# Kernel tuning notes

Hardware: AMD Instinct MI355X
Metric: run time of the kernel (lower is better)

Reference implementation:

```python
import jax, jax.numpy as jnp
import numpy as np

T, B, H, W, D, N, M, A = 48, 16, 16, 48, 684, 256, 256, 512
CQ, KQ, PAD = 512, 11, 5  # coverage conv: 1->512 channels, 11x11, pad 5


def setup_inputs() -> dict:
    key = jax.random.key(0)
    ks = iter(jax.random.split(key, 40))
    w = lambda *s: jax.random.normal(next(ks), s, jnp.float32) * 0.05
    inp = {
        "embedding": jax.random.normal(next(ks), (T, B, M), jnp.float32),
        "mask": jnp.ones((T, B), jnp.float32),
        "context": jax.random.normal(next(ks), (B, D, H, W), jnp.float32),
        "context_mask": jnp.ones((B, H, W), jnp.float32),
        "init_state": jax.random.normal(next(ks), (B, N), jnp.float32),
        # attention params
        "Ua_w": w(A, D), "Ua_b": w(A),              # conv_Ua (1x1 conv == linear over channels)
        "Wa_w": w(A, N),                              # fc_Wa (no bias)
        "Q_w": w(CQ, 1, KQ, KQ),                      # conv_Q (no bias)
        "Uf_w": w(A, CQ), "Uf_b": w(A),               # fc_Uf
        "va_w": w(1, A), "va_b": w(1),                # fc_va
        # GRU 1 (input-driven)
        "Wyz_w": w(N, M), "Wyz_b": w(N),
        "Wyr_w": w(N, M), "Wyr_b": w(N),
        "Wyh_w": w(N, M), "Wyh_b": w(N),
        "Uhz_w": w(N, N), "Uhr_w": w(N, N), "Uhh_w": w(N, N),
        # GRU 2 (context-driven)
        "Wcz_w": w(N, D), "Wcr_w": w(N, D), "Wch_w": w(N, D),
        "Uhz2_w": w(N, N), "Uhz2_b": w(N),
        "Uhr2_w": w(N, N), "Uhr2_b": w(N),
        "Uhh2_w": w(N, N), "Uhh2_b": w(N),
    }
    return inp


def reference(embedding, mask, context, context_mask, init_state,
              Ua_w, Ua_b, Wa_w, Q_w, Uf_w, Uf_b, va_w, va_b,
              Wyz_w, Wyz_b, Wyr_w, Wyr_b, Wyh_w, Wyh_b,
              Uhz_w, Uhr_w, Uhh_w, Wcz_w, Wcr_w, Wch_w,
              Uhz2_w, Uhz2_b, Uhr2_w, Uhr2_b, Uhh2_w, Uhh2_b):
    # Precompute, as the torch module does, the context projection and
    # embedding projections for all steps.
    Ua_ctx = jnp.einsum('bdhw,ad->hwba', context, Ua_w) + Ua_b   # [H,W,B,A]
    sz = jnp.einsum('tbm,nm->tbn', embedding, Wyz_w) + Wyz_b     # [T,B,N]
    sr = jnp.einsum('tbm,nm->tbn', embedding, Wyr_w) + Wyr_b
    sh = jnp.einsum('tbm,nm->tbn', embedding, Wyh_w) + Wyh_b
    ctx_mask_hwb = jnp.transpose(context_mask, (1, 2, 0))        # [H,W,B]
    nb = context.shape[0]
    alpha_past0 = jnp.zeros((nb, context.shape[2], context.shape[3]), context.dtype)

    def step(carry, xs):
        h, ap = carry
        m_t, sz_t, sr_t, sh_t = xs
        # GRU 1
        z1 = jax.nn.sigmoid(h @ Uhz_w.T + sz_t)
        r1 = jax.nn.sigmoid(h @ Uhr_w.T + sr_t)
        h1p = jnp.tanh((h @ Uhh_w.T) * r1 + sh_t)
        h1 = z1 * h + (1.0 - z1) * h1p
        h1 = m_t[:, None] * h1 + (1.0 - m_t)[:, None] * h
        # coverage-conv attention
        Wa_h1 = h1 @ Wa_w.T                                      # [B,A]
        cf = jax.lax.conv_general_dilated(
            ap[:, None], Q_w, (1, 1), [(PAD, PAD), (PAD, PAD)],
            dimension_numbers=('NCHW', 'OIHW', 'NCHW'))          # [B,CQ,H,W]
        cover = jnp.einsum('bchw,ac->hwba', cf, Uf_w) + Uf_b     # [H,W,B,A]
        att = jnp.tanh(Ua_ctx + Wa_h1[None, None] + cover)
        e = jnp.einsum('hwba,a->hwb', att, va_w[0]) + va_b[0]
        alpha = jnp.exp(e) * ctx_mask_hwb
        alpha = alpha / alpha.sum(axis=(0, 1))[None, None, :]    # normalize over H,W
        a_bhw = jnp.transpose(alpha, (2, 0, 1))
        ap_new = ap + a_bhw
        ct = jnp.einsum('bdhw,bhw->bd', context, a_bhw)          # [B,D]
        # GRU 2
        z2 = jax.nn.sigmoid(ct @ Wcz_w.T + h1 @ Uhz2_w.T + Uhz2_b)
        r2 = jax.nn.sigmoid(ct @ Wcr_w.T + h1 @ Uhr2_w.T + Uhr2_b)
        h2p = jnp.tanh(ct @ Wch_w.T + (h1 @ Uhh2_w.T + Uhh2_b) * r2)
        h2 = z2 * h1 + (1.0 - z2) * h2p
        h2 = m_t[:, None] * h2 + (1.0 - m_t)[:, None] * h1
        return (h2, ap_new), (h2, ct, a_bhw, ap_new)

    _, (h2ts, cts, alphas, alpha_pasts) = jax.lax.scan(
        step, (init_state, alpha_past0), (mask, sz, sr, sh))
    return h2ts, cts, alphas, alpha_pasts
```

## Files before the change

### kernel.cpp

```cpp
#include <hip/hip_runtime.h>
#include <hip/hip_bf16.h>
#include <stdint.h>

#define T_  48
#define B_  16
#define HW_ 768
#define D_  684
#define N_  256
#define A_  512

#define OFF_SZ     0u
#define OFF_SR     196608u
#define OFF_SH     393216u
#define OFF_UHZT   589824u
#define OFF_UHZ2T  786432u
#define OFF_G2HP   983040u
#define OFF_WAT    1179648u
#define OFF_WCZT   1310720u
#define OFF_UAB    1836032u
#define OFF_WAHP   2012160u
#define OFF_H1     2077696u
#define OFF_KCB    2186240u
#define OFF_G2CT   2219008u
#define OFF_AP     2275008u
#define OFF_AUN    2287296u
#define OFF_UACTX  2299584u

#define OUT_H2 0u
#define OUT_CT 196608u
#define OUT_AL 721920u
#define OUT_AP 1311744u

typedef __attribute__((ext_vector_type(8))) short bf16x8;
typedef __attribute__((ext_vector_type(16))) float floatx16;

__device__ __forceinline__ float sigf(float x)  { return 1.f / (1.f + __expf(-x)); }
__device__ __forceinline__ float tanhf_(float x){ float e = __expf(2.f*x); return 1.f - 2.f/(e + 1.f); }
__device__ __forceinline__ float bfval(unsigned short u){ return __uint_as_float(((unsigned)u) << 16); }
__device__ __forceinline__ unsigned short f2bf(float f){
  unsigned int x = __float_as_uint(f);
  return (unsigned short)((x + 0x7fffu + ((x >> 16) & 1u)) >> 16);
}

__global__ void k_prep(const float* __restrict__ Uhz, const float* __restrict__ Uhr, const float* __restrict__ Uhh,
                       const float* __restrict__ Uhz2, const float* __restrict__ Uhr2, const float* __restrict__ Uhh2,
                       const float* __restrict__ Wyz, const float* __restrict__ Wyr, const float* __restrict__ Wyh,
                       const float* __restrict__ Wa, const float* __restrict__ Wcz, const float* __restrict__ Wcr,
                       const float* __restrict__ Wch, const float* __restrict__ Ua, float* __restrict__ ws)
{
  int i = blockIdx.x * 256 + threadIdx.x;
  if (i < 589824) {
    int m = i >> 16, rem = i & 65535, r = rem >> 8, c = rem & 255;
    const float* s;
    unsigned dst;
    switch (m) { case 0: s=Uhz;  dst=OFF_UHZT;           break;
                 case 1: s=Uhr;  dst=OFF_UHZT+65536u;    break;
                 case 2: s=Uhh;  dst=OFF_UHZT+131072u;   break;
                 case 3: s=Uhz2; dst=OFF_UHZ2T;          break;
                 case 4: s=Uhr2; dst=OFF_UHZ2T+65536u;   break;
                 case 5: s=Uhh2; dst=OFF_UHZ2T+131072u;  break;
                 case 6: s=Wyz;  dst=983040u;            break;
                 case 7: s=Wyr;  dst=1048576u;           break;
                 default: s=Wyh; dst=1114112u;           break;}
    ws[dst + c*256 + r] = s[rem];
  } else if (i < 720896) {
    int j = i - 589824, r = j >> 8, c = j & 255;
    ws[OFF_WAT + c*512 + r] = Wa[j];
  } else if (i < 1246208) {
    int j = i - 720896; int m = j / 175104; int rem = j - m*175104;
    int r = rem / 684, c = rem - r*684;
    const float* s = (m == 0) ? Wcz : (m == 1) ? Wcr : Wch;
    ws[OFF_WCZT + m*175104 + c*256 + r] = s[rem];
  } else if (i < 1596416) {
    int j = i - 1246208; int a = j / 684, d = j - a*684;
    unsigned short* uab = (unsigned short*)(ws + OFF_UAB);
    uab[(size_t)a*688 + d] = f2bf(Ua[j]);
  } else if (i < 1598464) {
    int j = i - 1596416; int a = j >> 2, d = 684 + (j & 3);
    unsigned short* uab = (unsigned short*)(ws + OFF_UAB);
    uab[(size_t)a*688 + d] = 0;
  } else if (i < 1610752) {
    ws[OFF_AP + (i - 1598464)] = 0.f;
  }
}

__global__ void __launch_bounds__(256) k_kcomb(const float* __restrict__ Uf, const float* __restrict__ Qw,
                                               float* __restrict__ ws)
{
  unsigned short* kcb = (unsigned short*)(ws + OFF_KCB);
  int tid = threadIdx.x;
  int k = tid & 127, rr = tid >> 7;
  int a = blockIdx.x * 2 + rr;
  if (k >= 121) { kcb[(size_t)a*128 + k] = 0; return; }
  const float* uf = Uf + (size_t)a*512;
  float acc = 0.f;
  #pragma unroll 8
  for (int c = 0; c < 512; ++c) acc += uf[c] * Qw[c*121 + k];
  kcb[(size_t)a*128 + k] = f2bf(acc);
}

__global__ void k_embproj(const float* __restrict__ emb, const float* __restrict__ bz,
                          const float* __restrict__ br, const float* __restrict__ bh,
                          float* __restrict__ ws)
{
  __shared__ __align__(16) float s_e[256 * 16];
  int tid = threadIdx.x, row0 = blockIdx.x * 16;
  for (int i = tid; i < 4096; i += 256) { int r = i >> 8, m = i & 255; s_e[m*16 + r] = emb[(row0 + r)*256 + m]; }
  __syncthreads();
  int n = tid;
  float az[16], arr[16], ahh[16];
  float vz = bz[n], vr = br[n], vh = bh[n];
  #pragma unroll
  for (int r = 0; r < 16; ++r) { az[r] = vz; arr[r] = vr; ahh[r] = vh; }
  for (int m = 0; m < 256; ++m) {
    float wz = ws[983040u + m*256 + n];
    float wr = ws[1048576u + m*256 + n];
    float wh = ws[1114112u + m*256 + n];
    #pragma unroll
    for (int r = 0; r < 16; ++r) { float e = s_e[m*16 + r]; az[r] += wz*e; arr[r] += wr*e; ahh[r] += wh*e; }
  }
  #pragma unroll
  for (int r = 0; r < 16; ++r) {
    int ro = (row0 + r)*256 + n;
    ws[OFF_SZ + ro] = az[r]; ws[OFF_SR + ro] = arr[r]; ws[OFF_SH + ro] = ahh[r];
  }
}

__global__ void __launch_bounds__(256) k_uactx(const float* __restrict__ ctx, float* __restrict__ ws)
{
  __shared__ unsigned short sA[32 * 24];
  int tid = threadIdx.x;
  int blk = blockIdx.x;
  int b = blk / 48; int r2 = blk % 48; int ch = r2 >> 1; int ah = r2 & 1;
  int hw0 = ch * 32;
  const unsigned short* uab = (const unsigned short*)(ws + OFF_UAB);
  int lane = tid & 63, w = tid >> 6;
  int c5 = lane & 31, q = lane >> 5;
  int nb = ah*256 + w*64;
  floatx16 acc[2];
  #pragma unroll
  for (int nt = 0; nt < 2; ++nt)
    #pragma unroll
    for (int r = 0; r < 16; ++r) acc[nt][r] = 0.f;
  int dd = tid >> 4, iw = tid & 15;
  for (int kt = 0; kt < 43; ++kt) {
    int d = kt*16 + dd;
    float2 v = {0.f, 0.f};
    if (d < 684) v = *(const float2*)(ctx + ((size_t)(b*684 + d))*768 + hw0 + iw*2);
    __syncthreads();
    sA[(iw*2 + 0)*24 + dd] = f2bf(v.x);
    sA[(iw*2 + 1)*24 + dd] = f2bf(v.y);
    __syncthreads();
    bf16x8 af = *(const bf16x8*)(sA + c5*24 + q*8);
    #pragma unroll
    for (int nt = 0; nt < 2; ++nt) {
      bf16x8 bf = *(const bf16x8*)(uab + (size_t)(nb + nt*32 + c5)*688 + kt*16 + q*8);
      acc[nt] = __builtin_amdgcn_mfma_f32_32x32x16_bf16(af, bf, acc[nt], 0, 0, 0);
    }
  }
  unsigned short* up = (unsigned short*)(ws + OFF_UACTX);
  #pragma unroll
  for (int nt = 0; nt < 2; ++nt) {
    int col = nb + nt*32 + c5;
    #pragma unroll
    for (int r = 0; r < 16; ++r) {
      int row32 = (r & 3) + 8*(r >> 2) + 4*q;
      int hw = hw0 + row32;
      up[((size_t)(b*768 + hw))*512 + col] = f2bf(acc[nt][r]);
    }
  }
}

__global__ void __launch_bounds__(256) k_step0(const float* __restrict__ inits, const float* __restrict__ maskp,
                                               float* __restrict__ ws)
{
  __shared__ float s_h[256];
  __shared__ float s_part[3][8][32];
  __shared__ float s_h1[32];
  int tid = threadIdx.x;
  int b = blockIdx.x >> 3, q = blockIdx.x & 7;
  s_h[tid] = inits[b*256 + tid];
  if (q == 0) {
    for (int i = tid; i < 768; i += 256) ws[OFF_AUN + b*768 + i] = 0.f;
    #pragma unroll
    for (int g = 0; g < 3; ++g) ws[OFF_G2CT + (b*3 + g)*256 + tid] = 0.f;
  }
  __syncthreads();
  {
    int nl = tid & 31, kq = tid >> 5;
    int col = q*32 + nl;
    const float* Wz = ws + OFF_UHZT;
    const float* Wr = ws + OFF_UHZT + 65536u;
    const float* Wh = ws + OFF_UHZT + 131072u;
    float a0 = 0.f, a1 = 0.f, a2 = 0.f;
    #pragma unroll 8
    for (int k = kq*32; k < kq*32 + 32; ++k) {
      float hk = s_h[k];
      a0 += Wz[k*256 + col]*hk; a1 += Wr[k*256 + col]*hk; a2 += Wh[k*256 + col]*hk;
    }
    s_part[0][kq][nl] = a0; s_part[1][kq][nl] = a1; s_part[2][kq][nl] = a2;
  }
  __syncthreads();
  if (tid < 32) {
    float g0 = 0.f, g1 = 0.f, g2 = 0.f;
    #pragma unroll
    for (int j = 0; j < 8; ++j) { g0 += s_part[0][j][tid]; g1 += s_part[1][j][tid]; g2 += s_part[2][j][tid]; }
    int col = q*32 + tid;
    int ro = b*256 + col;
    float z1 = sigf(g0 + ws[OFF_SZ + ro]);
    float r1 = sigf(g1 + ws[OFF_SR + ro]);
    float h1p = tanhf_(g2 * r1 + ws[OFF_SH + ro]);
    float m = maskp[b];
    float h = s_h[col];
    float h1 = m*(z1*h + (1.f - z1)*h1p) + (1.f - m)*h;
    s_h1[tid] = h1;
    ws[OFF_H1 + b*256 + col] = h1;
  }
  __syncthreads();
  {
    float acc0 = 0.f, acc1 = 0.f;
    #pragma unroll 8
    for (int j = 0; j < 32; ++j) {
      float h1j = s_h1[j];
      acc0 += ws[OFF_WAT + (q*32 + j)*512 + tid]       * h1j;
      acc1 += ws[OFF_WAT + (q*32 + j)*512 + tid + 256] * h1j;
    }
    ws[OFF_WAHP + (size_t)(b*8 + q)*512 + tid]       = acc0;
    ws[OFF_WAHP + (size_t)(b*8 + q)*512 + tid + 256] = acc1;
  }
  #pragma unroll
  for (int g = 0; g < 3; ++g) {
    const float* Wb = ws + OFF_UHZ2T + g*65536u;
    float acc = 0.f;
    #pragma unroll 8
    for (int j = 0; j < 32; ++j) acc += Wb[(q*32 + j)*256 + tid] * s_h1[j];
    ws[OFF_G2HP + (size_t)((b*8 + q)*3 + g)*256 + tid] = acc;
  }
}

__global__ void __launch_bounds__(256) k_step1(int t, const float* __restrict__ maskp,
                                               const float* __restrict__ bz2, const float* __restrict__ br2,
                                               const float* __restrict__ bh2,
                                               float* __restrict__ out, float* __restrict__ ws)
{
  __shared__ float s_h[256];
  __shared__ float s_part[3][8][32];
  __shared__ float s_h1[32];
  int tid = threadIdx.x;
  int b = blockIdx.x >> 3, q = blockIdx.x & 7;
  const unsigned pr = (unsigned)((t - 1) & 1);
  const unsigned pw = (unsigned)(t & 1);
  {
    int n = tid;
    float h1v = ws[OFF_H1 + pr*4096u + b*256 + n];
    float gz = ws[OFF_G2CT + pr*12288u + (b*3 + 0)*256 + n];
    float gr = ws[OFF_G2CT + pr*12288u + (b*3 + 1)*256 + n];
    float gc = ws[OFF_G2CT + pr*12288u + (b*3 + 2)*256 + n];
    float gu = 0.f;
    #pragma unroll
    for (int qq = 0; qq < 8; ++qq) {
      gz += ws[OFF_G2HP + pr*98304u + (size_t)((b*8 + qq)*3 + 0)*256 + n];
      gr += ws[OFF_G2HP + pr*98304u + (size_t)((b*8 + qq)*3 + 1)*256 + n];
      gu += ws[OFF_G2HP + pr*98304u + (size_t)((b*8 + qq)*3 + 2)*256 + n];
    }
    float z2 = sigf(gz + bz2[n]);
    float r2 = sigf(gr + br2[n]);
    float h2p = tanhf_(gc + (gu + bh2[n]) * r2);
    float h2 = z2*h1v + (1.f - z2)*h2p;
    float m = maskp[(t-1)*16 + b];
    float hv = m*h2 + (1.f - m)*h1v;
    if (q == 0) out[OUT_H2 + (size_t)((t-1)*16 + b)*256 + n] = hv;
    s_h[n] = hv;
  }
  if (q == 0) {
    for (int i = tid; i < 768; i += 256) ws[OFF_AUN + b*768 + i] = 0.f;
    #pragma unroll
    for (int g = 0; g < 3; ++g) ws[OFF_G2CT + pw*12288u + (b*3 + g)*256 + tid] = 0.f;
  }
  __syncthreads();
  {
    int nl = tid & 31, kq = tid >> 5;
    int col = q*32 + nl;
    const float* Wz = ws + OFF_UHZT;
    const float* Wr = ws + OFF_UHZT + 65536u;
    const float* Wh = ws + OFF_UHZT + 131072u;
    float a0 = 0.f, a1 = 0.f, a2 = 0.f;
    #pragma unroll 8
    for (int k = kq*32; k < kq*32 + 32; ++k) {
      float hk = s_h[k];
      a0 += Wz[k*256 + col]*hk; a1 += Wr[k*256 + col]*hk; a2 += Wh[k*256 + col]*hk;
    }
    s_part[0][kq][nl] = a0; s_part[1][kq][nl] = a1; s_part[2][kq][nl] = a2;
  }
  __syncthreads();
  if (tid < 32) {
    float g0 = 0.f, g1 = 0.f, g2 = 0.f;
    #pragma unroll
    for (int j = 0; j < 8; ++j) { g0 += s_part[0][j][tid]; g1 += s_part[1][j][tid]; g2 += s_part[2][j][tid]; }
    int col = q*32 + tid;
    int ro = (t*16 + b)*256 + col;
    float z1 = sigf(g0 + ws[OFF_SZ + ro]);
    float r1 = sigf(g1 + ws[OFF_SR + ro]);
    float h1p = tanhf_(g2 * r1 + ws[OFF_SH + ro]);
    float m = maskp[t*16 + b];
    float h = s_h[col];
    float h1 = m*(z1*h + (1.f - z1)*h1p) + (1.f - m)*h;
    s_h1[tid] = h1;
    ws[OFF_H1 + pw*4096u + b*256 + col] = h1;
  }
  __syncthreads();
  {
    float acc0 = 0.f, acc1 = 0.f;
    #pragma unroll 8
    for (int j = 0; j < 32; ++j) {
      float h1j = s_h1[j];
      acc0 += ws[OFF_WAT + (q*32 + j)*512 + tid]       * h1j;
      acc1 += ws[OFF_WAT + (q*32 + j)*512 + tid + 256] * h1j;
    }
    ws[OFF_WAHP + (size_t)(b*8 + q)*512 + tid]       = acc0;
    ws[OFF_WAHP + (size_t)(b*8 + q)*512 + tid + 256] = acc1;
  }
  #pragma unroll
  for (int g = 0; g < 3; ++g) {
    const float* Wb = ws + OFF_UHZ2T + g*65536u;
    float acc = 0.f;
    #pragma unroll 8
    for (int j = 0; j < 32; ++j) acc += Wb[(q*32 + j)*256 + tid] * s_h1[j];
    ws[OFF_G2HP + pw*98304u + (size_t)((b*8 + q)*3 + g)*256 + tid] = acc;
  }
}

__global__ void __launch_bounds__(256) k_cover(const float* __restrict__ va,
                                               const float* __restrict__ Uab, const float* __restrict__ Ufb,
                                               float* __restrict__ ws)
{
  __shared__ unsigned short sA[64 * 136];
  __shared__ float sWah[512];
  __shared__ float sVa[512];
  int tid = threadIdx.x;
  int blk = blockIdx.x;
  int b = blk / 24; int chA = blk % 24; int mt = chA >> 1; int nt2 = chA & 1;
  for (int i = tid; i < 512; i += 256) {
    float v = Uab[i] + Ufb[i];
    #pragma unroll
    for (int qq = 0; qq < 8; ++qq) v += ws[OFF_WAHP + (size_t)(b*8 + qq)*512 + i];
    sWah[i] = v; sVa[i] = va[i];
  }
  const float* ap = ws + OFF_AP + b*768;
  for (int idx = tid; idx < 64*128; idx += 256) {
    int r = idx & 63, k = idx >> 6;
    int hw = mt*64 + r; int hh = hw / 48; int wwp = hw - hh*48;
    float v = 0.f;
    if (k < 121) {
      int kh = k / 11, kw = k - kh*11;
      int shh = hh + kh - 5, sww = wwp + kw - 5;
      if (shh >= 0 && shh < 16 && sww >= 0 && sww < 48) v = ap[shh*48 + sww];
    }
    sA[r*136 + k] = f2bf(v);
  }
  __syncthreads();
  int lane = tid & 63; int w = tid >> 6; int mw = w >> 1; int nw = w & 1;
  int c5 = lane & 31; int q = lane >> 5;
  bf16x8 af[8];
  {
    int m = mw*32 + c5;
    #pragma unroll
    for (int ks = 0; ks < 8; ++ks)
      af[ks] = *(const bf16x8*)(sA + m*136 + ks*16 + q*8);
  }
  const unsigned short* kct = (const unsigned short*)(ws + OFF_KCB);
  const unsigned short* uact = (const unsigned short*)(ws + OFF_UACTX);
  float e_part[16];
  #pragma unroll
  for (int r = 0; r < 16; ++r) e_part[r] = 0.f;
  for (int sp = 0; sp < 2; ++sp) {
    int n_base = nt2*256 + nw*128 + sp*64;
    floatx16 acc[2];
    #pragma unroll
    for (int r = 0; r < 16; ++r) { acc[0][r] = 0.f; acc[1][r] = 0.f; }
    const bf16x8* kb0 = (const bf16x8*)(kct + (size_t)(n_base + c5)*128 + q*8);
    const bf16x8* kb1 = (const bf16x8*)(kct + (size_t)(n_base + 32 + c5)*128 + q*8);
    #pragma unroll
    for (int ks = 0; ks < 8; ++ks) {
      bf16x8 b0 = kb0[ks*2];
      bf16x8 b1 = kb1[ks*2];
      acc[0] = __builtin_amdgcn_mfma_f32_32x32x16_bf16(af[ks], b0, acc[0], 0, 0, 0);
      acc[1] = __builtin_amdgcn_mfma_f32_32x32x16_bf16(af[ks], b1, acc[1], 0, 0, 0);
    }
    #pragma unroll
    for (int half = 0; half < 2; ++half) {
      int col = n_base + half*32 + c5;
      float vav = sVa[col], wah = sWah[col];
      #pragma unroll
      for (int r = 0; r < 16; ++r) {
        int row32 = (r & 3) + 8*(r >> 2) + 4*q;
        int hw = mt*64 + mw*32 + row32;
        float x = acc[half][r] + wah + bfval(uact[((size_t)(b*768 + hw))*512 + col]);
        e_part[r] += vav * tanhf_(x);
      }
    }
  }
  #pragma unroll
  for (int r = 0; r < 16; ++r) {
    float v = e_part[r];
    v += __shfl_xor(v, 1); v += __shfl_xor(v, 2); v += __shfl_xor(v, 4);
    v += __shfl_xor(v, 8); v += __shfl_xor(v, 16);
    e_part[r] = v;
  }
  if (c5 == 0) {
    #pragma unroll
    for (int r = 0; r < 16; ++r) {
      int row32 = (r & 3) + 8*(r >> 2) + 4*q;
      int hw = mt*64 + mw*32 + row32;
      atomicAdd(&ws[OFF_AUN + b*768 + hw], e_part[r]);
    }
  }
}

__global__ void __launch_bounds__(256) k_alpha(int t, const float* __restrict__ ctx, const float* __restrict__ cmask,
                                               const float* __restrict__ vab,
                                               float* __restrict__ out, float* __restrict__ ws)
{
  __shared__ __align__(16) float s_al[768];
  __shared__ float s_red[4];
  __shared__ float s_ct[32];
  int tid = threadIdx.x;
  int b = blockIdx.x / 22, dc = blockIdx.x % 22;
  const unsigned pw = (unsigned)(t & 1);
  float vb = vab[0];
  float local = 0.f;
  for (int i = tid; i < 768; i += 256) {
    float e = ws[OFF_AUN + b*768 + i] + vb;
    float un = __expf(e) * cmask[b*768 + i];
    s_al[i] = un; local += un;
  }
  local += __shfl_xor(local, 1); local += __shfl_xor(local, 2); local += __shfl_xor(local, 4);
  local += __shfl_xor(local, 8); local += __shfl_xor(local, 16); local += __shfl_xor(local, 32);
  if ((tid & 63) == 0) s_red[tid >> 6] = local;
  __syncthreads();
  float inv = 1.f / (s_red[0] + s_red[1] + s_red[2] + s_red[3]);
  if (dc == 0) {
    float* outA = out + OUT_AL + (size_t)(t*16 + b)*768;
    float* outP = out + OUT_AP + (size_t)(t*16 + b)*768;
    for (int i = tid; i < 768; i += 256) {
      float av = s_al[i] * inv;
      float np = ws[OFF_AP + b*768 + i] + av;
      ws[OFF_AP + b*768 + i] = np;
      outA[i] = av; outP[i] = np;
    }
  }
  {
    int dl = tid >> 3, qq = tid & 7;
    int d = dc*32 + dl;
    if (d < 684) {
      const float4* cp  = (const float4*)(ctx + ((size_t)(b*684 + d))*768);
      const float4* alp = (const float4*)s_al;
      float s = 0.f;
      #pragma unroll 8
      for (int i = 0; i < 24; ++i) {
        float4 cv = cp[i*8 + qq]; float4 av = alp[i*8 + qq];
        s += cv.x*av.x + cv.y*av.y + cv.z*av.z + cv.w*av.w;
      }
      s += __shfl_xor(s, 1); s += __shfl_xor(s, 2); s += __shfl_xor(s, 4);
      s *= inv;
      if (qq == 0) {
        out[OUT_CT + (size_t)(t*16 + b)*684 + d] = s;
        s_ct[dl] = s;
      }
    } else if (qq == 0) {
      s_ct[dl] = 0.f;
    }
  }
  __syncthreads();
  {
    int d0 = dc*32;
    int jm = 684 - d0; if (jm > 32) jm = 32;
    #pragma unroll
    for (int g = 0; g < 3; ++g) {
      const float* Wb = ws + OFF_WCZT + g*175104u;
      float acc = 0.f;
      for (int j = 0; j < jm; ++j) acc += Wb[(d0 + j)*256 + tid] * s_ct[j];
      atomicAdd(&ws[OFF_G2CT + pw*12288u + (size_t)(b*3 + g)*256 + tid], acc);
    }
  }
}

__global__ void k_final(const float* __restrict__ maskp, const float* __restrict__ bz2,
                        const float* __restrict__ br2, const float* __restrict__ bh2,
                        float* __restrict__ out, float* __restrict__ ws)
{
  int b = blockIdx.x, n = threadIdx.x;
  const unsigned pr = 1u;
  float h1v = ws[OFF_H1 + pr*4096u + b*256 + n];
  float gz = ws[OFF_G2CT + pr*12288u + (b*3 + 0)*256 + n];
  float gr = ws[OFF_G2CT + pr*12288u + (b*3 + 1)*256 + n];
  float gc = ws[OFF_G2CT + pr*12288u + (b*3 + 2)*256 + n];
  float gu = 0.f;
  #pragma unroll
  for (int qq = 0; qq < 8; ++qq) {
    gz += ws[OFF_G2HP + pr*98304u + (size_t)((b*8 + qq)*3 + 0)*256 + n];
    gr += ws[OFF_G2HP + pr*98304u + (size_t)((b*8 + qq)*3 + 1)*256 + n];
    gu += ws[OFF_G2HP + pr*98304u + (size_t)((b*8 + qq)*3 + 2)*256 + n];
  }
  float z2 = sigf(gz + bz2[n]);
  float r2 = sigf(gr + br2[n]);
  float h2p = tanhf_(gc + (gu + bh2[n]) * r2);
  float h2 = z2*h1v + (1.f - z2)*h2p;
  float m = maskp[47*16 + b];
  out[OUT_H2 + (size_t)(47*16 + b)*256 + n] = m*h2 + (1.f - m)*h1v;
}

extern "C" void kernel_launch(void* const* d_in, const int* in_sizes, int n_in,
                              void* d_out, int out_size, void* d_ws, size_t ws_size,
                              hipStream_t stream)
{
  const float* emb   = (const float*)d_in[0];
  const float* maskp = (const float*)d_in[1];
  const float* ctx   = (const float*)d_in[2];
  const float* cmask = (const float*)d_in[3];
  const float* inits = (const float*)d_in[4];
  const float* Ua    = (const float*)d_in[5];
  const float* Uab   = (const float*)d_in[6];
  const float* Wa    = (const float*)d_in[7];
  const float* Qw    = (const float*)d_in[8];
  const float* Uf    = (const float*)d_in[9];
  const float* Ufb   = (const float*)d_in[10];
  const float* va    = (const float*)d_in[11];
  const float* vab   = (const float*)d_in[12];
  const float* Wyz   = (const float*)d_in[13];
  const float* Wyzb  = (const float*)d_in[14];
  const float* Wyr   = (const float*)d_in[15];
  const float* Wyrb  = (const float*)d_in[16];
  const float* Wyh   = (const float*)d_in[17];
  const float* Wyhb  = (const float*)d_in[18];
  const float* Uhz   = (const float*)d_in[19];
  const float* Uhr   = (const float*)d_in[20];
  const float* Uhh   = (const float*)d_in[21];
  const float* Wcz   = (const float*)d_in[22];
  const float* Wcr   = (const float*)d_in[23];
  const float* Wch   = (const float*)d_in[24];
  const float* Uhz2  = (const float*)d_in[25];
  const float* Uhz2b = (const float*)d_in[26];
  const float* Uhr2  = (const float*)d_in[27];
  const float* Uhr2b = (const float*)d_in[28];
  const float* Uhh2  = (const float*)d_in[29];
  const float* Uhh2b = (const float*)d_in[30];
  float* out = (float*)d_out;
  float* ws  = (float*)d_ws;

  k_prep<<<dim3(6292), dim3(256), 0, stream>>>(Uhz, Uhr, Uhh, Uhz2, Uhr2, Uhh2,
                                               Wyz, Wyr, Wyh, Wa, Wcz, Wcr, Wch, Ua, ws);
  k_kcomb<<<dim3(256), dim3(256), 0, stream>>>(Uf, Qw, ws);
  k_embproj<<<dim3(48), dim3(256), 0, stream>>>(emb, Wyzb, Wyrb, Wyhb, ws);
  k_uactx<<<dim3(768), dim3(256), 0, stream>>>(ctx, ws);
  k_step0<<<dim3(128), dim3(256), 0, stream>>>(inits, maskp, ws);

  k_cover<<<dim3(384), dim3(256), 0, stream>>>(va, Uab, Ufb, ws);
  k_alpha<<<dim3(352), dim3(256), 0, stream>>>(0, ctx, cmask, vab, out, ws);
  for (int t = 1; t < 48; ++t) {
    k_step1<<<dim3(128), dim3(256), 0, stream>>>(t, maskp, Uhz2b, Uhr2b, Uhh2b, out, ws);
    k_cover<<<dim3(384), dim3(256), 0, stream>>>(va, Uab, Ufb, ws);
    k_alpha<<<dim3(352), dim3(256), 0, stream>>>(t, ctx, cmask, vab, out, ws);
  }
  k_final<<<dim3(16), dim3(256), 0, stream>>>(maskp, Uhz2b, Uhr2b, Uhh2b, out, ws);
  (void)in_sizes; (void)n_in; (void)out_size; (void)ws_size;
}
```

Baseline: 2.505 ms.

## Split embedding projection across column tiles and K-groups with shared-memory reduction

The embedding projection kernel goes from 48 blocks to 384 blocks. Each block now covers 32 output columns, and the 256-long inner dimension is split across 8 warp groups. Partial sums are reduced through shared memory and the bias is added at the end. The embedding reads are also vectorised as float4. The aim is to fill the GPU better in a one-time prologue kernel, at the cost of extra shared memory and a second sync.

```diff
diff --git a/kernel.cpp b/kernel.cpp
--- a/kernel.cpp
+++ b/kernel.cpp
@@ -99,30 +99,57 @@
   kcb[(size_t)a*128 + k] = f2bf(acc);
 }
 
-__global__ void k_embproj(const float* __restrict__ emb, const float* __restrict__ bz,
-                          const float* __restrict__ br, const float* __restrict__ bh,
-                          float* __restrict__ ws)
+__global__ void __launch_bounds__(256) k_embproj(const float* __restrict__ emb, const float* __restrict__ bz,
+                                                 const float* __restrict__ br, const float* __restrict__ bh,
+                                                 float* __restrict__ ws)
 {
   __shared__ __align__(16) float s_e[256 * 16];
-  int tid = threadIdx.x, row0 = blockIdx.x * 16;
+  __shared__ float s_part[8][32][48];
+  int tid = threadIdx.x;
+  int rc = blockIdx.x >> 3, cc = blockIdx.x & 7;
+  int row0 = rc * 16, n0 = cc * 32;
   for (int i = tid; i < 4096; i += 256) { int r = i >> 8, m = i & 255; s_e[m*16 + r] = emb[(row0 + r)*256 + m]; }
   __syncthreads();
-  int n = tid;
-  float az[16], arr[16], ahh[16];
-  float vz = bz[n], vr = br[n], vh = bh[n];
-  #pragma unroll
-  for (int r = 0; r < 16; ++r) { az[r] = vz; arr[r] = vr; ahh[r] = vh; }
-  for (int m = 0; m < 256; ++m) {
+  int col = tid & 31, kg = tid >> 5;
+  int n = n0 + col;
+  float az[16], ar[16], ah[16];
+  #pragma unroll
+  for (int r = 0; r < 16; ++r) { az[r] = 0.f; ar[r] = 0.f; ah[r] = 0.f; }
+  #pragma unroll 4
+  for (int m = kg*32; m < kg*32 + 32; ++m) {
     float wz = ws[983040u + m*256 + n];
     float wr = ws[1048576u + m*256 + n];
     float wh = ws[1114112u + m*256 + n];
-    #pragma unroll
-    for (int r = 0; r < 16; ++r) { float e = s_e[m*16 + r]; az[r] += wz*e; arr[r] += wr*e; ahh[r] += wh*e; }
+    const float4* ep = (const float4*)(s_e + m*16);
+    #pragma unroll
+    for (int rq = 0; rq < 4; ++rq) {
+      float4 e4 = ep[rq];
+      az[rq*4+0] += wz*e4.x; az[rq*4+1] += wz*e4.y; az[rq*4+2] += wz*e4.z; az[rq*4+3] += wz*e4.w;
+      ar[rq*4+0] += wr*e4.x; ar[rq*4+1] += wr*e4.y; ar[rq*4+2] += wr*e4.z; ar[rq*4+3] += wr*e4.w;
+      ah[rq*4+0] += wh*e4.x; ah[rq*4+1] += wh*e4.y; ah[rq*4+2] += wh*e4.z; ah[rq*4+3] += wh*e4.w;
+    }
   }
   #pragma unroll
   for (int r = 0; r < 16; ++r) {
-    int ro = (row0 + r)*256 + n;
-    ws[OFF_SZ + ro] = az[r]; ws[OFF_SR + ro] = arr[r]; ws[OFF_SH + ro] = ahh[r];
+    s_part[kg][col][r]      = az[r];
+    s_part[kg][col][16 + r] = ar[r];
+    s_part[kg][col][32 + r] = ah[r];
+  }
+  __syncthreads();
+  {
+    int rcol = tid & 31, j0 = (tid >> 5) * 6;
+    int rn = n0 + rcol;
+    #pragma unroll
+    for (int jj = 0; jj < 6; ++jj) {
+      int j = j0 + jj;
+      float v = 0.f;
+      #pragma unroll
+      for (int k8 = 0; k8 < 8; ++k8) v += s_part[k8][rcol][j];
+      int g = j >> 4, r = j & 15;
+      const float* bp = (g == 0) ? bz : (g == 1) ? br : bh;
+      v += bp[rn];
+      ws[g*196608u + (row0 + r)*256 + rn] = v;
+    }
   }
 }
 
@@ -551,7 +578,7 @@
   k_prep<<<dim3(6292), dim3(256), 0, stream>>>(Uhz, Uhr, Uhh, Uhz2, Uhr2, Uhh2,
                                                Wyz, Wyr, Wyh, Wa, Wcz, Wcr, Wch, Ua, ws);
   k_kcomb<<<dim3(256), dim3(256), 0, stream>>>(Uf, Qw, ws);
-  k_embproj<<<dim3(48), dim3(256), 0, stream>>>(emb, Wyzb, Wyrb, Wyhb, ws);
+  k_embproj<<<dim3(384), dim3(256), 0, stream>>>(emb, Wyzb, Wyrb, Wyhb, ws);
   k_uactx<<<dim3(768), dim3(256), 0, stream>>>(ctx, ws);
   k_step0<<<dim3(128), dim3(256), 0, stream>>>(inits, maskp, ws);
 
```

New measurement: 2.473 ms. No clear change (-1.3%).
